# Kernel optimization log

Hardware: AMD Instinct MI355X
Metric: run time of the kernel (lower is better)

Reference implementation:

```python
import jax, jax.numpy as jnp
import numpy as np
import math

B, T, D = 2, 4096, 2048
H, d_head, C = 16, 128, 64


def binarize(x):
    # sign to {-1,+1} with straight-through estimator (identity gradient)
    s = jnp.where(x >= 0, jnp.ones_like(x), -jnp.ones_like(x))
    return x + jax.lax.stop_gradient(s - x)


def setup_inputs() -> dict:
    key = jax.random.key(0)
    ks = jax.random.split(key, 5)
    w_std = 1.0 / math.sqrt(D)
    return {
        "x": jax.random.normal(ks[0], (B, T, D), dtype=jnp.float32),
        "Wq": jax.random.normal(ks[1], (D, D), dtype=jnp.float32) * w_std,
        "Wk": jax.random.normal(ks[2], (D, D), dtype=jnp.float32) * w_std,
        "Wv": jax.random.normal(ks[3], (D, D), dtype=jnp.float32) * w_std,
        "Wo": jax.random.normal(ks[4], (D, D), dtype=jnp.float32) * w_std,
    }


def reference(x, Wq, Wk, Wv, Wo):
    Bx, Tx, Dx = x.shape
    scale = 1.0 / math.sqrt(d_head)
    # projections (torch Linear: y = x @ W.T), split heads -> [B,H,T,d]
    q = (x @ Wq.T).reshape(Bx, Tx, H, d_head).transpose(0, 2, 1, 3) * scale
    k = binarize((x @ Wk.T).reshape(Bx, Tx, H, d_head).transpose(0, 2, 1, 3))
    v = binarize((x @ Wv.T).reshape(Bx, Tx, H, d_head).transpose(0, 2, 1, 3))
    N = Tx // C  # T chosen divisible by chunk_size
    qc = q.reshape(Bx, H, N, C, d_head)
    kc = k.reshape(Bx, H, N, C, d_head)
    vc = v.reshape(Bx, H, N, C, d_head)
    # intra-chunk causal attention
    mask = jnp.tril(jnp.ones((C, C), dtype=x.dtype))
    intra_scores = jnp.einsum('bhnid,bhnjd->bhnij', qc, kc) * mask
    intra = jnp.einsum('bhnij,bhnjd->bhnid', intra_scores, vc)
    # cross-chunk: exclusive prefix sum of per-chunk k^T v outer products
    chunk_kv = jnp.einsum('bhnci,bhncj->bhnij', kc, vc)  # [B,H,N,d,d]
    cs = jnp.cumsum(chunk_kv, axis=2)
    prefix = cs - chunk_kv  # exclusive cumsum
    cross = jnp.einsum('bhncd,bhnde->bhnce', qc, prefix)
    output = (intra + cross).reshape(Bx, H, Tx, d_head)
    out = output.transpose(0, 2, 1, 3).reshape(Bx, Tx, Dx) @ Wo.T
    final_state = cs[:, :, -1]  # [B,H,d,d]
    return out, final_state
```

## Files before the change

kernel.cpp:

```cpp
#include <hip/hip_runtime.h>
#include <stdint.h>

typedef __attribute__((ext_vector_type(8))) short short8;
typedef __attribute__((ext_vector_type(4))) float f32x4;
typedef unsigned short u16;

__device__ __forceinline__ u16 f2bf(float f) {
  uint32_t u = __builtin_bit_cast(uint32_t, f);
  u = (u + 0x7FFFu + ((u >> 16) & 1u)) >> 16;
  return (u16)u;
}
__device__ __forceinline__ float bf2f(u16 h) {
  uint32_t u = ((uint32_t)h) << 16;
  return __builtin_bit_cast(float, u);
}
__device__ __forceinline__ void lds16(const u16* g, u16* l) {
  __builtin_amdgcn_global_load_lds(
      (const __attribute__((address_space(1))) void*)g,
      (__attribute__((address_space(3))) void*)l, 16, 0, 0);
}
__device__ __forceinline__ int sw256(int i) { return i ^ (((i >> 7) & 7) << 3); }
__device__ __forceinline__ int sw128(int i) { return i ^ (((i >> 6) & 7) << 3); }
__device__ __forceinline__ int swzA64(int i) { return i ^ (((i >> 6) & 7) << 3); }
__device__ __forceinline__ int swzA32(int i) { return i ^ (((i >> 6) & 3) << 3); }

__global__ void split_kernel(const float* __restrict__ in, u16* __restrict__ hi,
                             u16* __restrict__ lo, int n) {
  int i = blockIdx.x * blockDim.x + threadIdx.x;
  int stride = gridDim.x * blockDim.x;
  for (; i < n; i += stride) {
    float v = in[i];
    u16 h = f2bf(v);
    hi[i] = h;
    if (lo) lo[i] = f2bf(v - bf2f(h));
  }
}

template<int SPLIT, int EPI>
__global__ __launch_bounds__(512, 2) void gemm8p(
    const u16* __restrict__ Ahi, const u16* __restrict__ Alo,
    const u16* __restrict__ Bhi, const u16* __restrict__ Blo,
    u16* __restrict__ outb, float* __restrict__ outf,
    int Mdim, int Ndim, int Kdim)
{
  constexpr int BK   = (SPLIT > 1) ? 32 : 64;
  constexpr int KS   = BK / 32;
  constexpr int TILE = 256 * BK;
  constexpr int NMAT = (SPLIT > 1) ? 4 : 2;
  constexpr int AOFF_H = 0;
  constexpr int AOFF_L = (SPLIT > 1) ? TILE : 0;
  constexpr int BOFF_H = (SPLIT > 1) ? 2*TILE : TILE;
  constexpr int BOFF_L = (SPLIT > 1) ? 3*TILE : 0;
  __shared__ __align__(16) u16 smem[2 * NMAT * TILE];

  const int t = threadIdx.x, l = t & 63, w = t >> 6;
  const int wm = w >> 2, wn = w & 3;
  const int fr = l & 15, fs = l >> 4;
  const int sb = (blockIdx.x & 7) * 32 + (blockIdx.x >> 3);
  const int m0 = (sb >> 3) * 256, n0 = (sb & 7) * 256;
  const int NT = Kdim / BK;

#define SWZ(i) ((BK == 64) ? swzA64(i) : swzA32(i))

  auto STAGE = [&](int unit, int kt) {
    if (kt >= NT) return;
    const int bufb = (kt & 1) * NMAT * TILE;
    const int k0 = kt * BK;
    const bool isB = unit & 1;
    const int odd = unit >> 1;
    const int g0 = isB ? n0 : m0;
    if constexpr (SPLIT == 1) {
      const u16* src = isB ? Bhi : Ahi;
      const int mb = bufb + (isB ? BOFF_H : AOFF_H);
#pragma unroll
      for (int i = 0; i < 2; i++) {
        int L = i * 512 + t;
        int d = isB ? (((L >> 8) << 12) + ((L & 255) << 3) + (odd << 11))
                    : (((L >> 9) << 13) + ((L & 511) << 3) + (odd << 12));
        int r = d >> 6, s = (d >> 3) & 7;
        lds16(src + (size_t)(g0 + r) * Kdim + k0 + ((s ^ (r & 7)) << 3), smem + mb + d);
      }
    } else {
      const u16* sh = isB ? Bhi : Ahi;
      const u16* sl = isB ? Blo : Alo;
      const int mh = bufb + (isB ? BOFF_H : AOFF_H);
      int d = isB ? (((t >> 7) << 11) + ((t & 127) << 3) + (odd << 10))
                  : (((t >> 8) << 12) + ((t & 255) << 3) + (odd << 11));
      int r = d >> 5, s = (d >> 3) & 3;
      size_t g = (size_t)(g0 + r) * Kdim + k0 + ((s ^ ((r >> 1) & 3)) << 3);
      lds16(sh + g, smem + mh + d);
      lds16(sl + g, smem + mh + TILE + d);
    }
  };

  f32x4 acc[8][4] = {};

#define PHASE(KT, Q, UNIT, SKT, VM) {                                          \
  const int bufb_ = ((KT) & 1) * NMAT * TILE;                                  \
  short8 rah[4][KS], ral[4][KS], rbh[2][KS], rbl[2][KS];                       \
  _Pragma("unroll") for (int fm = 0; fm < 4; fm++)                             \
    _Pragma("unroll") for (int ks = 0; ks < KS; ks++) {                        \
      int ia = (wm*128 + ((Q)>>1)*64 + fm*16 + fr)*BK + ks*32 + fs*8;          \
      rah[fm][ks] = *(const short8*)(smem + bufb_ + AOFF_H + SWZ(ia));         \
      if constexpr (SPLIT > 1)                                                 \
        ral[fm][ks] = *(const short8*)(smem + bufb_ + AOFF_L + SWZ(ia));       \
    }                                                                          \
  _Pragma("unroll") for (int fn = 0; fn < 2; fn++)                             \
    _Pragma("unroll") for (int ks = 0; ks < KS; ks++) {                        \
      int ib = (wn*64 + ((Q)&1)*32 + fn*16 + fr)*BK + ks*32 + fs*8;            \
      rbh[fn][ks] = *(const short8*)(smem + bufb_ + BOFF_H + SWZ(ib));         \
      if constexpr (SPLIT > 1)                                                 \
        rbl[fn][ks] = *(const short8*)(smem + bufb_ + BOFF_L + SWZ(ib));       \
    }                                                                          \
  STAGE((UNIT), (SKT));                                                        \
  if constexpr (VM) {                                                          \
    if ((SKT) < NT) asm volatile("s_waitcnt vmcnt(4)" ::: "memory");           \
    else            asm volatile("s_waitcnt vmcnt(0)" ::: "memory");           \
  }                                                                            \
  __builtin_amdgcn_s_barrier();                                                \
  asm volatile("s_waitcnt lgkmcnt(0)" ::: "memory");                           \
  __builtin_amdgcn_sched_barrier(0);                                           \
  __builtin_amdgcn_s_setprio(1);                                               \
  _Pragma("unroll") for (int fm = 0; fm < 4; fm++)                             \
    _Pragma("unroll") for (int fn = 0; fn < 2; fn++)                           \
      _Pragma("unroll") for (int ks = 0; ks < KS; ks++) {                      \
        f32x4& A = acc[((Q)>>1)*4 + fm][((Q)&1)*2 + fn];                       \
        A = __builtin_amdgcn_mfma_f32_16x16x32_bf16(rah[fm][ks], rbh[fn][ks], A, 0,0,0); \
        if constexpr (SPLIT > 1) {                                             \
          A = __builtin_amdgcn_mfma_f32_16x16x32_bf16(rah[fm][ks], rbl[fn][ks], A, 0,0,0); \
          A = __builtin_amdgcn_mfma_f32_16x16x32_bf16(ral[fm][ks], rbh[fn][ks], A, 0,0,0); \
        }                                                                      \
      }                                                                        \
  __builtin_amdgcn_s_setprio(0);                                               \
  __builtin_amdgcn_sched_barrier(0);                                           \
  __builtin_amdgcn_s_barrier();                                                \
}

  STAGE(0, 0); STAGE(1, 0); STAGE(2, 0); STAGE(3, 0);
  STAGE(0, 1); STAGE(1, 1);
  asm volatile("s_waitcnt vmcnt(4)" ::: "memory");
  __builtin_amdgcn_s_barrier();

  const int LI = NT >> 1;
  for (int i = 0; i < LI; i++) {
    const int Ta = 2*i, Tb = 2*i + 1;
    PHASE(Ta, 0, 2, Tb,   0)
    PHASE(Ta, 1, 3, Tb,   0)
    PHASE(Ta, 2, 0, Ta+2, 0)
    PHASE(Ta, 3, 1, Ta+2, 1)
    PHASE(Tb, 0, 2, Ta+2, 0)
    PHASE(Tb, 1, 3, Ta+2, 0)
    PHASE(Tb, 2, 0, Tb+2, 0)
    PHASE(Tb, 3, 1, Tb+2, 1)
  }
#undef PHASE
#undef SWZ

  const float qscale = 0.08838834764831843f;
#pragma unroll
  for (int fm = 0; fm < 8; fm++)
#pragma unroll
    for (int fn = 0; fn < 4; fn++)
#pragma unroll
      for (int r = 0; r < 4; r++) {
        int gm = m0 + wm*128 + fm*16 + fs*4 + r;
        int gn = n0 + wn*64 + fn*16 + fr;
        float val = acc[fm][fn][r];
        if constexpr (EPI == 2) {
          outf[(size_t)gm * Ndim + gn] = val;
        } else {
          int b = gm >> 12, tt = gm & 4095, h = gn >> 7, dd = gn & 127;
          size_t idx = (((size_t)(b*16 + h))*4096 + tt)*128 + dd;
          if constexpr (EPI == 0) outb[idx] = f2bf(val * qscale);
          else                    outb[idx] = (val >= 0.f) ? (u16)0x3F80 : (u16)0xBF80;
        }
      }
}

__global__ void pack_signs(const u16* __restrict__ k, const u16* __restrict__ v,
                           unsigned long long* __restrict__ kp, unsigned long long* __restrict__ vp) {
  const int blk = blockIdx.x;
  const int d = threadIdx.x;
  const int bh = blk >> 6, n = blk & 63;
  size_t base = (((size_t)bh * 4096) + n * 64) * 128 + d;
  unsigned long long kw = 0, vw = 0;
  for (int c = 0; c < 64; c++) {
    kw |= (unsigned long long)(k[base + (size_t)c*128] >> 15) << c;
    vw |= (unsigned long long)(v[base + (size_t)c*128] >> 15) << c;
  }
  kp[(size_t)blk * 128 + d] = kw;
  vp[(size_t)blk * 128 + d] = vw;
}

__global__ __launch_bounds__(256) void scan_kernel(
    const unsigned long long* __restrict__ kp, const unsigned long long* __restrict__ vp,
    short* __restrict__ pfx8, float* __restrict__ fsT)
{
  const int t = threadIdx.x;
  const int bh = blockIdx.x >> 6, ep = blockIdx.x & 63;
  const int e = ep * 2 + (t >> 7), d = t & 127;
  const size_t base = (size_t)bh * 64 * 128;
  int s = 0;
  for (int n = 0; n < 64; n++) {
    if ((n & 7) == 0)
      pfx8[((size_t)(bh*8 + (n>>3))*128 + e)*128 + d] = (short)s;
    unsigned long long kw = kp[base + (size_t)n*128 + d];
    unsigned long long vw = vp[base + (size_t)n*128 + e];
    s += 64 - 2*__popcll(kw ^ vw);
  }
  fsT[((size_t)bh*128 + e)*128 + d] = (float)s;
}

__global__ __launch_bounds__(256) void transpose_fs(const float* __restrict__ fsT,
                                                    float* __restrict__ fstate) {
  __shared__ float tile[32*130];
  const int t = threadIdx.x;
  const int bh = blockIdx.x >> 2, es = (blockIdx.x & 3) * 32;
#pragma unroll
  for (int i = 0; i < 16; i++) {
    int idx = t + i*256;
    int e2 = idx >> 7, d = idx & 127;
    tile[e2*130 + d] = fsT[((size_t)bh*128 + es + e2)*128 + d];
  }
  __syncthreads();
#pragma unroll
  for (int i = 0; i < 16; i++) {
    int idx = t + i*256;
    int d = idx >> 5, e2 = idx & 31;
    fstate[((size_t)bh*128 + d)*128 + es + e2] = tile[e2*130 + d];
  }
}

__global__ __launch_bounds__(256) void fused_attn(
    const u16* __restrict__ q, const u16* __restrict__ k,
    const unsigned long long* __restrict__ kp, const unsigned long long* __restrict__ vp,
    const short* __restrict__ pfx8, u16* __restrict__ att)
{
  __shared__ __align__(16) u16 smem[28672];
  u16* sQ  = smem;
  u16* sP1 = smem + 8192;
  u16* sP2 = smem + 16384;
  u16* sS  = smem + 24576;

  const int t = threadIdx.x, l = t & 63, w = t >> 6;
  const int blk = blockIdx.x, bh = blk >> 6, n = blk & 63;
  const int b = bh >> 4, hh = bh & 15;
  const int fr = l & 15, fs = l >> 4;
  const size_t qbase = (((size_t)bh * 4096) + n * 64) * 128;
  const size_t pbase = (size_t)bh * 64 * 128;

#pragma unroll
  for (int i = 0; i < 4; i++) {
    int arow = i*16 + (t>>4);
    int aslot = (t & 15) ^ (arow & 7);
    size_t g = qbase + (size_t)arow*128 + aslot*8;
    lds16(q + g, sQ + i*2048 + t*8);
    lds16(k + g, sP1 + i*2048 + t*8);
  }
  {
    int d = t >> 1, ch = (t & 1) * 32;
    unsigned long long wv = vp[pbase + (size_t)n*128 + d];
#pragma unroll
    for (int c = 0; c < 32; c += 2) {
      uint32_t b0 = ((wv >> (ch + c)) & 1ull)     ? 0xBF80u : 0x3F80u;
      uint32_t b1 = ((wv >> (ch + c + 1)) & 1ull) ? 0xBF80u : 0x3F80u;
      int li = d*64 + ch + c;
      *(uint32_t*)(sP2 + sw128(li)) = b0 | (b1 << 16);
    }
  }
  __syncthreads();

  f32x4 accS[4] = {};
#pragma unroll
  for (int kk = 0; kk < 4; kk++) {
    int la = (w*16 + fr)*128 + kk*32 + fs*8;
    short8 a = *(const short8*)(sQ + sw256(la));
#pragma unroll
    for (int fn = 0; fn < 4; fn++) {
      int lb = (fn*16 + fr)*128 + kk*32 + fs*8;
      short8 bb = *(const short8*)(sP1 + sw256(lb));
      accS[fn] = __builtin_amdgcn_mfma_f32_16x16x32_bf16(a, bb, accS[fn], 0, 0, 0);
    }
  }
#pragma unroll
  for (int fn = 0; fn < 4; fn++)
#pragma unroll
    for (int r = 0; r < 4; r++) {
      int i = w*16 + fs*4 + r, j = fn*16 + fr;
      float v = (j <= i) ? accS[fn][r] : 0.f;
      sS[sw128(i*64 + j)] = f2bf(v);
    }
  __syncthreads();

  f32x4 accI[8] = {};
#pragma unroll
  for (int kk = 0; kk < 2; kk++) {
    int la = (w*16 + fr)*64 + kk*32 + fs*8;
    short8 a = *(const short8*)(sS + sw128(la));
#pragma unroll
    for (int fn = 0; fn < 8; fn++) {
      int lb = (fn*16 + fr)*64 + kk*32 + fs*8;
      short8 bb = *(const short8*)(sP2 + sw128(lb));
      accI[fn] = __builtin_amdgcn_mfma_f32_16x16x32_bf16(a, bb, accI[fn], 0, 0, 0);
    }
  }
  __syncthreads();

  const int m0 = n & ~7, cnt = n & 7;
  for (int hf = 0; hf < 2; hf++) {
#pragma unroll
    for (int p = 0; p < 4; p++) {
      int erow = p*16 + (t>>4);
      int e = hf*64 + erow;
      const short* ps = pfx8 + ((size_t)(bh*8 + (n>>3))*128 + e)*128 + (t&15)*8;
      short8 pv = *(const short8*)ps;
      int accj[8];
#pragma unroll
      for (int j = 0; j < 8; j++) accj[j] = pv[j];
      for (int m = 0; m < cnt; m++) {
        unsigned long long vw = vp[pbase + (size_t)(m0+m)*128 + e];
#pragma unroll
        for (int j = 0; j < 8; j++) {
          unsigned long long kw = kp[pbase + (size_t)(m0+m)*128 + (t&15)*8 + j];
          accj[j] += 64 - 2*__popcll(kw ^ vw);
        }
      }
      short8 hi, lo;
#pragma unroll
      for (int j = 0; j < 8; j++) {
        hi[j] = (short)f2bf((float)(accj[j] >> 5));
        lo[j] = (short)f2bf((float)(accj[j] & 31));
      }
      int pi = sw256(erow*128 + (t&15)*8);
      *(short8*)(sP1 + pi) = hi;
      *(short8*)(sP2 + pi) = lo;
    }
    __syncthreads();

    f32x4 acch[4] = {}, accl[4] = {};
#pragma unroll
    for (int kk = 0; kk < 4; kk++) {
      int la = (w*16 + fr)*128 + kk*32 + fs*8;
      short8 a = *(const short8*)(sQ + sw256(la));
#pragma unroll
      for (int fn = 0; fn < 4; fn++) {
        int pb = sw256((fn*16 + fr)*128 + kk*32 + fs*8);
        acch[fn] = __builtin_amdgcn_mfma_f32_16x16x32_bf16(a, *(const short8*)(sP1 + pb), acch[fn], 0, 0, 0);
        accl[fn] = __builtin_amdgcn_mfma_f32_16x16x32_bf16(a, *(const short8*)(sP2 + pb), accl[fn], 0, 0, 0);
      }
    }
#pragma unroll
    for (int fn = 0; fn < 4; fn++)
#pragma unroll
      for (int r = 0; r < 4; r++) {
        int c = w*16 + fs*4 + r;
        int dcol = hf*64 + fn*16 + fr;
        float val = accI[hf*4+fn][r] + 32.f*acch[fn][r] + accl[fn][r];
        size_t idx = ((size_t)(b*4096 + n*64 + c))*2048 + hh*128 + dcol;
        att[idx] = f2bf(val);
      }
    __syncthreads();
  }
}

extern "C" void kernel_launch(void* const* d_in, const int* in_sizes, int n_in,
                              void* d_out, int out_size, void* d_ws, size_t ws_size,
                              hipStream_t stream) {
  (void)in_sizes; (void)n_in; (void)out_size; (void)ws_size;
  const float* x  = (const float*)d_in[0];
  const float* Wq = (const float*)d_in[1];
  const float* Wk = (const float*)d_in[2];
  const float* Wv = (const float*)d_in[3];
  const float* Wo = (const float*)d_in[4];
  float* out = (float*)d_out;
  float* fstate = out + (size_t)16777216;

  char* ws = (char*)d_ws;
  u16* x_hi = (u16*)(ws + 0);
  u16* x_lo = (u16*)(ws + 33554432);
  u16* qb   = (u16*)(ws + 67108864);
  u16* kb   = (u16*)(ws + 100663296);
  u16* vb   = (u16*)(ws + 134217728);
  u16* wq_h = (u16*)(ws + 167772160);
  u16* wk_h = (u16*)(ws + 176160768);
  u16* wk_l = (u16*)(ws + 184549376);
  u16* wv_h = (u16*)(ws + 192937984);
  u16* wv_l = (u16*)(ws + 201326592);
  u16* wo_h = (u16*)(ws + 209715200);
  unsigned long long* kpk = (unsigned long long*)(ws + 218103808);
  unsigned long long* vpk = (unsigned long long*)(ws + 220200960);
  u16* att    = x_hi;
  float* fsT  = (float*)(ws + 33554432);
  short* pfx8 = (short*)(ws + 134217728);

  split_kernel<<<2048, 256, 0, stream>>>(x,  x_hi, x_lo, 16777216);
  split_kernel<<<1024, 256, 0, stream>>>(Wq, wq_h, nullptr, 4194304);
  split_kernel<<<1024, 256, 0, stream>>>(Wk, wk_h, wk_l, 4194304);
  split_kernel<<<1024, 256, 0, stream>>>(Wv, wv_h, wv_l, 4194304);
  split_kernel<<<1024, 256, 0, stream>>>(Wo, wo_h, nullptr, 4194304);

  gemm8p<1,0><<<256, 512, 0, stream>>>(x_hi, nullptr, wq_h, nullptr, qb, nullptr, 8192, 2048, 2048);
  gemm8p<3,1><<<256, 512, 0, stream>>>(x_hi, x_lo, wk_h, wk_l, kb, nullptr, 8192, 2048, 2048);
  gemm8p<3,1><<<256, 512, 0, stream>>>(x_hi, x_lo, wv_h, wv_l, vb, nullptr, 8192, 2048, 2048);

  pack_signs<<<2048, 128, 0, stream>>>(kb, vb, kpk, vpk);
  scan_kernel<<<2048, 256, 0, stream>>>(kpk, vpk, pfx8, fsT);
  transpose_fs<<<128, 256, 0, stream>>>(fsT, fstate);
  fused_attn<<<2048, 256, 0, stream>>>(qb, kb, kpk, vpk, pfx8, att);

  gemm8p<1,2><<<256, 512, 0, stream>>>(att, nullptr, wo_h, nullptr, nullptr, out, 8192, 2048, 2048);
}
```

Baseline: 750.0 us.

## Restructure GEMM main loop into one barrier per k-tile with full-tile fragment loads

```diff
diff --git a/kernel.cpp b/kernel.cpp
--- a/kernel.cpp
+++ b/kernel.cpp
@@ -23,6 +23,8 @@
 __device__ __forceinline__ int sw128(int i) { return i ^ (((i >> 6) & 7) << 3); }
 __device__ __forceinline__ int swzA64(int i) { return i ^ (((i >> 6) & 7) << 3); }
 __device__ __forceinline__ int swzA32(int i) { return i ^ (((i >> 6) & 3) << 3); }
+
+#define SB0() __builtin_amdgcn_sched_barrier(0)
 
 __global__ void split_kernel(const float* __restrict__ in, u16* __restrict__ hi,
                              u16* __restrict__ lo, int n) {
@@ -44,7 +46,6 @@
     int Mdim, int Ndim, int Kdim)
 {
   constexpr int BK   = (SPLIT > 1) ? 32 : 64;
-  constexpr int KS   = BK / 32;
   constexpr int TILE = 256 * BK;
   constexpr int NMAT = (SPLIT > 1) ? 4 : 2;
   constexpr int AOFF_H = 0;
@@ -62,98 +63,103 @@
 
 #define SWZ(i) ((BK == 64) ? swzA64(i) : swzA32(i))
 
-  auto STAGE = [&](int unit, int kt) {
+  auto STAGE = [&](int kt) {
     if (kt >= NT) return;
     const int bufb = (kt & 1) * NMAT * TILE;
     const int k0 = kt * BK;
-    const bool isB = unit & 1;
-    const int odd = unit >> 1;
-    const int g0 = isB ? n0 : m0;
+#pragma unroll
+    for (int unit = 0; unit < 4; unit++) {
+      const bool isB = unit & 1;
+      const int odd = unit >> 1;
+      const int g0 = isB ? n0 : m0;
+      if constexpr (SPLIT == 1) {
+        const u16* src = isB ? Bhi : Ahi;
+        const int mb = bufb + (isB ? BOFF_H : AOFF_H);
+#pragma unroll
+        for (int i = 0; i < 2; i++) {
+          int L = i * 512 + t;
+          int d = isB ? (((L >> 8) << 12) + ((L & 255) << 3) + (odd << 11))
+                      : (((L >> 9) << 13) + ((L & 511) << 3) + (odd << 12));
+          int r = d >> 6, s = (d >> 3) & 7;
+          lds16(src + (size_t)(g0 + r) * Kdim + k0 + ((s ^ (r & 7)) << 3), smem + mb + d);
+        }
+      } else {
+        const u16* sh = isB ? Bhi : Ahi;
+        const u16* sl = isB ? Blo : Alo;
+        const int mh = bufb + (isB ? BOFF_H : AOFF_H);
+        int d = isB ? (((t >> 7) << 11) + ((t & 127) << 3) + (odd << 10))
+                    : (((t >> 8) << 12) + ((t & 255) << 3) + (odd << 11));
+        int r = d >> 5, s = (d >> 3) & 3;
+        size_t g = (size_t)(g0 + r) * Kdim + k0 + ((s ^ ((r >> 1) & 3)) << 3);
+        lds16(sh + g, smem + mh + d);
+        lds16(sl + g, smem + mh + TILE + d);
+      }
+    }
+  };
+
+  f32x4 acc[8][4] = {};
+
+  auto RD_A = [&](short8* dst, int bufb, int off, int ks) {
+#pragma unroll
+    for (int fm = 0; fm < 8; fm++) {
+      int ia = (wm*128 + fm*16 + fr)*BK + ks*32 + fs*8;
+      dst[fm] = *(const short8*)(smem + bufb + off + SWZ(ia));
+    }
+  };
+  auto RD_B = [&](short8* dst, int bufb, int off, int ks) {
+#pragma unroll
+    for (int fn = 0; fn < 4; fn++) {
+      int ib = (wn*64 + fn*16 + fr)*BK + ks*32 + fs*8;
+      dst[fn] = *(const short8*)(smem + bufb + off + SWZ(ib));
+    }
+  };
+  auto PASS = [&](const short8* ra, const short8* rb) {
+    __builtin_amdgcn_s_setprio(1);
+#pragma unroll
+    for (int fm = 0; fm < 8; fm++)
+#pragma unroll
+      for (int fn = 0; fn < 4; fn++)
+        acc[fm][fn] = __builtin_amdgcn_mfma_f32_16x16x32_bf16(ra[fm], rb[fn], acc[fm][fn], 0, 0, 0);
+    __builtin_amdgcn_s_setprio(0);
+  };
+
+  STAGE(0);
+  asm volatile("s_waitcnt vmcnt(0)" ::: "memory");
+  __builtin_amdgcn_s_barrier();
+
+  for (int T = 0; T < NT; T++) {
+    const int bufb = (T & 1) * NMAT * TILE;
     if constexpr (SPLIT == 1) {
-      const u16* src = isB ? Bhi : Ahi;
-      const int mb = bufb + (isB ? BOFF_H : AOFF_H);
-#pragma unroll
-      for (int i = 0; i < 2; i++) {
-        int L = i * 512 + t;
-        int d = isB ? (((L >> 8) << 12) + ((L & 255) << 3) + (odd << 11))
-                    : (((L >> 9) << 13) + ((L & 511) << 3) + (odd << 12));
-        int r = d >> 6, s = (d >> 3) & 7;
-        lds16(src + (size_t)(g0 + r) * Kdim + k0 + ((s ^ (r & 7)) << 3), smem + mb + d);
-      }
+      short8 a0[8], b0[4], a1[8], b1[4];
+      RD_A(a0, bufb, AOFF_H, 0); RD_B(b0, bufb, BOFF_H, 0);
+      SB0();
+      STAGE(T + 1);
+      RD_A(a1, bufb, AOFF_H, 1); RD_B(b1, bufb, BOFF_H, 1);
+      SB0();
+      asm volatile("s_waitcnt lgkmcnt(12)" ::: "memory"); SB0();
+      PASS(a0, b0); SB0();
+      asm volatile("s_waitcnt lgkmcnt(0)" ::: "memory"); SB0();
+      PASS(a1, b1); SB0();
+      asm volatile("s_waitcnt vmcnt(0)" ::: "memory");
+      __builtin_amdgcn_s_barrier();
     } else {
-      const u16* sh = isB ? Bhi : Ahi;
-      const u16* sl = isB ? Blo : Alo;
-      const int mh = bufb + (isB ? BOFF_H : AOFF_H);
-      int d = isB ? (((t >> 7) << 11) + ((t & 127) << 3) + (odd << 10))
-                  : (((t >> 8) << 12) + ((t & 255) << 3) + (odd << 11));
-      int r = d >> 5, s = (d >> 3) & 3;
-      size_t g = (size_t)(g0 + r) * Kdim + k0 + ((s ^ ((r >> 1) & 3)) << 3);
-      lds16(sh + g, smem + mh + d);
-      lds16(sl + g, smem + mh + TILE + d);
-    }
-  };
-
-  f32x4 acc[8][4] = {};
-
-#define PHASE(KT, Q, UNIT, SKT, VM) {                                          \
-  const int bufb_ = ((KT) & 1) * NMAT * TILE;                                  \
-  short8 rah[4][KS], ral[4][KS], rbh[2][KS], rbl[2][KS];                       \
-  _Pragma("unroll") for (int fm = 0; fm < 4; fm++)                             \
-    _Pragma("unroll") for (int ks = 0; ks < KS; ks++) {                        \
-      int ia = (wm*128 + ((Q)>>1)*64 + fm*16 + fr)*BK + ks*32 + fs*8;          \
-      rah[fm][ks] = *(const short8*)(smem + bufb_ + AOFF_H + SWZ(ia));         \
-      if constexpr (SPLIT > 1)                                                 \
-        ral[fm][ks] = *(const short8*)(smem + bufb_ + AOFF_L + SWZ(ia));       \
-    }                                                                          \
-  _Pragma("unroll") for (int fn = 0; fn < 2; fn++)                             \
-    _Pragma("unroll") for (int ks = 0; ks < KS; ks++) {                        \
-      int ib = (wn*64 + ((Q)&1)*32 + fn*16 + fr)*BK + ks*32 + fs*8;            \
-      rbh[fn][ks] = *(const short8*)(smem + bufb_ + BOFF_H + SWZ(ib));         \
-      if constexpr (SPLIT > 1)                                                 \
-        rbl[fn][ks] = *(const short8*)(smem + bufb_ + BOFF_L + SWZ(ib));       \
-    }                                                                          \
-  STAGE((UNIT), (SKT));                                                        \
-  if constexpr (VM) {                                                          \
-    if ((SKT) < NT) asm volatile("s_waitcnt vmcnt(4)" ::: "memory");           \
-    else            asm volatile("s_waitcnt vmcnt(0)" ::: "memory");           \
-  }                                                                            \
-  __builtin_amdgcn_s_barrier();                                                \
-  asm volatile("s_waitcnt lgkmcnt(0)" ::: "memory");                           \
-  __builtin_amdgcn_sched_barrier(0);                                           \
-  __builtin_amdgcn_s_setprio(1);                                               \
-  _Pragma("unroll") for (int fm = 0; fm < 4; fm++)                             \
-    _Pragma("unroll") for (int fn = 0; fn < 2; fn++)                           \
-      _Pragma("unroll") for (int ks = 0; ks < KS; ks++) {                      \
-        f32x4& A = acc[((Q)>>1)*4 + fm][((Q)&1)*2 + fn];                       \
-        A = __builtin_amdgcn_mfma_f32_16x16x32_bf16(rah[fm][ks], rbh[fn][ks], A, 0,0,0); \
-        if constexpr (SPLIT > 1) {                                             \
-          A = __builtin_amdgcn_mfma_f32_16x16x32_bf16(rah[fm][ks], rbl[fn][ks], A, 0,0,0); \
-          A = __builtin_amdgcn_mfma_f32_16x16x32_bf16(ral[fm][ks], rbh[fn][ks], A, 0,0,0); \
-        }                                                                      \
-      }                                                                        \
-  __builtin_amdgcn_s_setprio(0);                                               \
-  __builtin_amdgcn_sched_barrier(0);                                           \
-  __builtin_amdgcn_s_barrier();                                                \
-}
-
-  STAGE(0, 0); STAGE(1, 0); STAGE(2, 0); STAGE(3, 0);
-  STAGE(0, 1); STAGE(1, 1);
-  asm volatile("s_waitcnt vmcnt(4)" ::: "memory");
-  __builtin_amdgcn_s_barrier();
-
-  const int LI = NT >> 1;
-  for (int i = 0; i < LI; i++) {
-    const int Ta = 2*i, Tb = 2*i + 1;
-    PHASE(Ta, 0, 2, Tb,   0)
-    PHASE(Ta, 1, 3, Tb,   0)
-    PHASE(Ta, 2, 0, Ta+2, 0)
-    PHASE(Ta, 3, 1, Ta+2, 1)
-    PHASE(Tb, 0, 2, Ta+2, 0)
-    PHASE(Tb, 1, 3, Ta+2, 0)
-    PHASE(Tb, 2, 0, Tb+2, 0)
-    PHASE(Tb, 3, 1, Tb+2, 1)
-  }
-#undef PHASE
+      short8 ah[8], bh_[4], al[8], bl[4];
+      RD_A(ah, bufb, AOFF_H, 0); RD_B(bh_, bufb, BOFF_H, 0);
+      SB0();
+      STAGE(T + 1);
+      RD_B(bl, bufb, BOFF_L, 0);
+      RD_A(al, bufb, AOFF_L, 0);
+      SB0();
+      asm volatile("s_waitcnt lgkmcnt(12)" ::: "memory"); SB0();
+      PASS(ah, bh_); SB0();
+      asm volatile("s_waitcnt lgkmcnt(8)" ::: "memory"); SB0();
+      PASS(ah, bl); SB0();
+      asm volatile("s_waitcnt lgkmcnt(0)" ::: "memory"); SB0();
+      PASS(al, bh_); SB0();
+      asm volatile("s_waitcnt vmcnt(0)" ::: "memory");
+      __builtin_amdgcn_s_barrier();
+    }
+  }
 #undef SWZ
 
   const float qscale = 0.08838834764831843f;
```

Measured after the change: 803.1 us. +7.1%, slower.
